# Kernel tuning notes

Measured on AMD Instinct MI355X. Metric: run time of the kernel, lower is better.

## Reference

```python
import jax, jax.numpy as jnp
import numpy as np

N = 524288   # total spokes
D = 128      # dim_hidden
B = 128      # graphs in batch
H = 64       # hubs per graph (static, num_hubs_type='S')
K = 4        # hubs_per_spoke


def setup_inputs() -> dict:
    key = jax.random.key(0)
    ks = jax.random.split(key, 5)
    x = jax.random.normal(ks[0], (N, D), jnp.float32)
    spoke_init_hub_idx = jax.random.randint(ks[1], (N,), 0, H)
    batch_idx = jnp.sort(jax.random.randint(ks[2], (N,), 0, B))
    s1 = 1.0 / np.sqrt(D)
    s2 = 1.0 / np.sqrt(2 * D)
    W1 = jax.random.uniform(ks[3], (D, 2 * D), jnp.float32, -s1, s1)
    b1 = jnp.zeros((2 * D,), jnp.float32)
    W2 = jax.random.uniform(ks[4], (2 * D, D), jnp.float32, -s2, s2)
    b2 = jnp.zeros((D,), jnp.float32)
    return {"x": x, "spoke_init_hub_idx": spoke_init_hub_idx, "batch_idx": batch_idx,
            "W1": W1, "b1": b1, "W2": W2, "b2": b2}


def reference(x, spoke_init_hub_idx, batch_idx, W1, b1, W2, b2):
    # FeedForward on spokes: Linear -> GELU(exact, torch default) -> Linear
    h = jax.nn.gelu(x @ W1 + b1, approximate=False) @ W2 + b2  # [N, D]

    # batched hub index: local hub idx offset by graph (uniform H hubs/graph)
    gidx = batch_idx * H + spoke_init_hub_idx  # [N]

    # scatter_mean of spoke features into hubs (empty hubs -> 0, as torch scatter_mean)
    sums = jax.ops.segment_sum(h, gidx, num_segments=B * H)                    # [B*H, D]
    cnt = jax.ops.segment_sum(jnp.ones((N,), h.dtype), gidx, num_segments=B * H)
    hub_features = sums / jnp.maximum(cnt, 1.0)[:, None]                       # [B*H, D]

    # assign each spoke to the K hubs closest to its initial hub (within its graph)
    hf = hub_features.reshape(B, H, D)
    d2 = jnp.sum((hf[:, :, None, :] - hf[:, None, :, :]) ** 2, axis=-1)        # [B, H, H]
    _, knn = jax.lax.top_k(-d2, K)                                             # [B, H, K] local hub ids
    hubs_idx = knn[batch_idx, spoke_init_hub_idx] + batch_idx[:, None] * H     # [N, K] global hub ids
    spokes_idx = jnp.repeat(jnp.arange(N), K)
    spokes_hubs_edge_index = jnp.stack([spokes_idx, hubs_idx.reshape(-1)], axis=0)  # [2, N*K]

    return hub_features, spokes_hubs_edge_index
```

## Files before the change

### kernel.cpp

```cpp
#include <hip/hip_runtime.h>
#include <hip/hip_bf16.h>

#define N_SPOKES 524288
#define DIM      128
#define DIM2     256
#define NB       128
#define NH       64
#define BH       8192

#define OUT_HF   0
#define OUT_E0   1048576
#define OUT_E1   3145728

typedef __attribute__((ext_vector_type(8))) short  short8;
typedef __attribute__((ext_vector_type(4))) float  float4v;
typedef __attribute__((ext_vector_type(4))) unsigned short ushort4v;

__device__ inline unsigned short f2bf(float f) {
    __hip_bfloat16 h = __float2bfloat16(f);
    return *reinterpret_cast<unsigned short*>(&h);
}

__device__ inline unsigned int pkbf(float a, float b) {
    __hip_bfloat162 h = __float22bfloat162_rn(make_float2(a, b));
    union { __hip_bfloat162 h; unsigned int u; } cv;
    cv.h = h;
    return cv.u;
}

__device__ inline float gelu_f(float v) {
    float s = v * (1.0f + 0.044715f * v * v);
    float e = __builtin_exp2f(-2.302118131f * s);
    return v * __builtin_amdgcn_rcpf(1.0f + e);
}

__global__ void setup_kernel(const int* __restrict__ batchidx, const int* __restrict__ hubidx,
                             const float* __restrict__ W1,
                             unsigned short* __restrict__ w1t,
                             int* __restrict__ goff, int* __restrict__ cnt) {
    int b = blockIdx.x, tid = threadIdx.x;
    if (b < 2048) {
        int i = b * 256 + tid;
        if (i < N_SPOKES) {
            int bi = batchidx[i];
            int bp = (i == 0) ? -1 : batchidx[i - 1];
            for (int g = bp + 1; g <= bi; ++g) goff[g] = i;
            if (i == N_SPOKES - 1)
                for (int g = bi + 1; g <= NB; ++g) goff[g] = N_SPOKES;
            atomicAdd(&cnt[bi * NH + hubidx[i]], 1);
        }
    } else {
        int idx = (b - 2048) * 256 + tid;
        if (idx < DIM * DIM2) {
            int n = idx >> 7, k = idx & 127;
            w1t[idx] = f2bf(W1[k * DIM2 + n]);
        }
    }
}

__launch_bounds__(512, 2)
__global__ void ffn_fused(const float* __restrict__ x,
                          const int* __restrict__ hubidx,
                          const int* __restrict__ goff,
                          const unsigned short* __restrict__ w1t,
                          const float* __restrict__ b1,
                          float* __restrict__ outbuf,
                          int atomic_mode) {
    __shared__ unsigned short sA[2][128 * 136];
    __shared__ unsigned short sU[256 * 40];
    __shared__ unsigned short sOne[2][64 * 136];

    const int tid  = threadIdx.x;
    const int lane = tid & 63;
    const int w    = tid >> 6;
    const int c_lo = lane & 15;
    const int c_hi = lane >> 4;
    const int wcb  = w * 32;
    const int g      = blockIdx.x >> 1;
    const int cchunk = blockIdx.x & 1;

    const int s = goff[g], e = goff[g + 1];
    const int len = e - s;
    const int cs  = (len + 1) >> 1;
    const int ms  = s + cchunk * cs;
    int me = ms + cs; if (me > e) me = e;
    const int n  = me - ms;
    const int nt = (n > 0) ? ((n + 127) >> 7) : 0;

    short8 bfr[2][4];
    #pragma unroll
    for (int n4 = 0; n4 < 2; ++n4)
        #pragma unroll
        for (int k = 0; k < 4; ++k) {
            int col = wcb + n4 * 16 + c_lo;
            bfr[n4][k] = *(const short8*)(w1t + col * DIM + k * 32 + c_hi * 8);
        }
    float bcol[2];
    #pragma unroll
    for (int n4 = 0; n4 < 2; ++n4) bcol[n4] = b1[wcb + n4 * 16 + c_lo];

    float4v hacc[4][2];
    #pragma unroll
    for (int mt = 0; mt < 4; ++mt)
        #pragma unroll
        for (int n4 = 0; n4 < 2; ++n4) hacc[mt][n4] = (float4v){0.f, 0.f, 0.f, 0.f};

    for (int i = tid; i < 4096; i += 512) {
        int b = i >> 11, r = (i >> 5) & 63, c = i & 31;
        *(unsigned long long*)&sOne[b][r * 136 + c * 4] = 0ULL;
    }

    const float4v* x4 = (const float4v*)x;

    float4v ld[8];
    int hub_nxt = -1;
    int hubA = -1, hubB = -1;
    if (nt > 0) {
        #pragma unroll
        for (int it = 0; it < 8; ++it) {
            int f = it * 512 + tid;
            int r = f >> 5;
            int rr = r < n ? r : n - 1;
            ld[it] = x4[(size_t)(ms + rr) * 32 + (f & 31)];
        }
        if (tid < 128) hub_nxt = (tid < n) ? hubidx[ms + tid] : -1;
    }
    __syncthreads();

    for (int t = 0; t < nt; ++t) {
        const int p = t & 1;
        const int hub_cur = hub_nxt;
        const int hclear  = p ? hubB : hubA;

        if (tid < 128) {
            if (hclear >= 0)  sOne[p][hclear * 136 + tid] = 0;
            if (hub_cur >= 0) sOne[p][hub_cur * 136 + tid] = (unsigned short)0x3F80;
        }
        if (p) hubB = hub_cur; else hubA = hub_cur;

        #pragma unroll
        for (int it = 0; it < 8; ++it) {
            int f = it * 512 + tid;
            int row = f >> 5, c4 = f & 31;
            float4v v = ld[it];
            unsigned int lo = pkbf(v.x, v.y);
            unsigned int hi = pkbf(v.z, v.w);
            *(uint2*)&sA[p][row * 136 + c4 * 4] = make_uint2(lo, hi);
        }
        __syncthreads();

        if (t + 1 < nt) {
            #pragma unroll
            for (int it = 0; it < 8; ++it) {
                int f = it * 512 + tid;
                int r = (t + 1) * 128 + (f >> 5);
                int rr = r < n ? r : n - 1;
                ld[it] = x4[(size_t)(ms + rr) * 32 + (f & 31)];
            }
            if (tid < 128) {
                int r = (t + 1) * 128 + tid;
                hub_nxt = (r < n) ? hubidx[ms + r] : -1;
            }
        }

        #pragma unroll
        for (int ks = 0; ks < 4; ++ks) {
            float4v acc[2][2];
            #pragma unroll
            for (int m2 = 0; m2 < 2; ++m2)
                #pragma unroll
                for (int n4 = 0; n4 < 2; ++n4) acc[m2][n4] = (float4v){0.f, 0.f, 0.f, 0.f};

            #pragma unroll
            for (int k = 0; k < 4; ++k)
                #pragma unroll
                for (int m2 = 0; m2 < 2; ++m2) {
                    short8 a = *(const short8*)&sA[p][(ks * 32 + m2 * 16 + c_lo) * 136 + k * 32 + c_hi * 8];
                    acc[m2][0] = __builtin_amdgcn_mfma_f32_16x16x32_bf16(a, bfr[0][k], acc[m2][0], 0, 0, 0);
                    acc[m2][1] = __builtin_amdgcn_mfma_f32_16x16x32_bf16(a, bfr[1][k], acc[m2][1], 0, 0, 0);
                }

            #pragma unroll
            for (int m2 = 0; m2 < 2; ++m2) {
                int rbase = m2 * 16 + c_hi * 4;
                #pragma unroll
                for (int n4 = 0; n4 < 2; ++n4) {
                    int col = wcb + n4 * 16 + c_lo;
                    float4v a4 = acc[m2][n4];
                    unsigned int lo = pkbf(gelu_f(a4.x + bcol[n4]), gelu_f(a4.y + bcol[n4]));
                    unsigned int hi = pkbf(gelu_f(a4.z + bcol[n4]), gelu_f(a4.w + bcol[n4]));
                    *(uint2*)&sU[col * 40 + rbase] = make_uint2(lo, hi);
                }
            }

            short8 aS[4];
            #pragma unroll
            for (int mt = 0; mt < 4; ++mt)
                aS[mt] = *(const short8*)&sOne[p][(mt * 16 + c_lo) * 136 + ks * 32 + c_hi * 8];
            short8 bU[2];
            #pragma unroll
            for (int n4 = 0; n4 < 2; ++n4)
                bU[n4] = *(const short8*)&sU[(wcb + n4 * 16 + c_lo) * 40 + c_hi * 8];
            #pragma unroll
            for (int mt = 0; mt < 4; ++mt)
                #pragma unroll
                for (int n4 = 0; n4 < 2; ++n4)
                    hacc[mt][n4] = __builtin_amdgcn_mfma_f32_16x16x32_bf16(aS[mt], bU[n4], hacc[mt][n4], 0, 0, 0);
        }
    }

    #pragma unroll
    for (int mt = 0; mt < 4; ++mt)
        #pragma unroll
        for (int n4 = 0; n4 < 2; ++n4) {
            float4v v = hacc[mt][n4];
            int col = wcb + n4 * 16 + c_lo;
            #pragma unroll
            for (int reg = 0; reg < 4; ++reg) {
                int hub = mt * 16 + c_hi * 4 + reg;
                size_t o = ((size_t)g * NH + hub) * DIM2 + col;
                if (atomic_mode) atomicAdd(&outbuf[o], v[reg]);
                else outbuf[(size_t)cchunk * BH * DIM2 + o] = v[reg];
            }
        }
}

__global__ void hubfeat_kernel(const float* __restrict__ part, int nchunk,
                               const int* __restrict__ cnt,
                               const float* __restrict__ W2, const float* __restrict__ b2,
                               float* __restrict__ out) {
    __shared__ float sSum[16 * 256];
    int tid = threadIdx.x;
    int d   = tid & 127;
    int hh  = tid >> 7;

    for (int i = tid; i < 16 * 256; i += 256) {
        size_t o = (size_t)(blockIdx.x * 16) * DIM2 + i;
        float v = 0.f;
        for (int c = 0; c < nchunk; ++c) v += part[(size_t)c * BH * DIM2 + o];
        sSum[i] = v;
    }
    __syncthreads();

    int h0 = hh * 8;
    float acc[8] = {0.f, 0.f, 0.f, 0.f, 0.f, 0.f, 0.f, 0.f};
    for (int k4 = 0; k4 < 64; ++k4) {
        float w0 = W2[(k4 * 4 + 0) * DIM + d];
        float w1 = W2[(k4 * 4 + 1) * DIM + d];
        float w2 = W2[(k4 * 4 + 2) * DIM + d];
        float w3 = W2[(k4 * 4 + 3) * DIM + d];
        #pragma unroll
        for (int j = 0; j < 8; ++j) {
            float4v sv = *(const float4v*)&sSum[(h0 + j) * 256 + k4 * 4];
            acc[j] += sv.x * w0 + sv.y * w1 + sv.z * w2 + sv.w * w3;
        }
    }
    float b2d = b2[d];
    #pragma unroll
    for (int j = 0; j < 8; ++j) {
        int h = blockIdx.x * 16 + h0 + j;
        float c = (float)cnt[h];
        out[OUT_HF + h * DIM + d] = (acc[j] + c * b2d) / fmaxf(c, 1.0f);
    }
}

__global__ void knn_edges(const float* __restrict__ hf, const int* __restrict__ goff,
                          const int* __restrict__ hubidx, float* __restrict__ out) {
    __shared__ float s[64 * 129];
    __shared__ float d2[64 * 64];
    __shared__ int sK[64 * 4];
    int g = blockIdx.x, tid = threadIdx.x;

    for (int i = tid; i < 64 * 128; i += 256) {
        int r = i >> 7, c = i & 127;
        s[r * 129 + c] = hf[OUT_HF + (g * 64 + r) * DIM + c];
    }
    __syncthreads();

    for (int p = tid; p < 4096; p += 256) {
        int i = p >> 6, j = p & 63;
        float a = 0.f;
        for (int k = 0; k < 128; ++k) {
            float dd = s[i * 129 + k] - s[j * 129 + k];
            a += dd * dd;
        }
        d2[p] = a;
    }
    __syncthreads();

    if (tid < 64) {
        float bv0 = 1e30f, bv1 = 1e30f, bv2 = 1e30f, bv3 = 1e30f;
        int   bi0 = 0,     bi1 = 0,     bi2 = 0,     bi3 = 0;
        for (int j = 0; j < 64; ++j) {
            float v = d2[tid * 64 + j];
            if (v < bv0)      { bv3=bv2; bi3=bi2; bv2=bv1; bi2=bi1; bv1=bv0; bi1=bi0; bv0=v; bi0=j; }
            else if (v < bv1) { bv3=bv2; bi3=bi2; bv2=bv1; bi2=bi1; bv1=v;   bi1=j; }
            else if (v < bv2) { bv3=bv2; bi3=bi2; bv2=v;   bi2=j; }
            else if (v < bv3) { bv3=v;   bi3=j; }
        }
        sK[tid * 4 + 0] = bi0; sK[tid * 4 + 1] = bi1;
        sK[tid * 4 + 2] = bi2; sK[tid * 4 + 3] = bi3;
    }
    __syncthreads();

    int sgs = goff[g], sge = goff[g + 1];
    float gbase = (float)(g * NH);
    for (int i = sgs + tid; i < sge; i += 256) {
        int h = hubidx[i];
        int4 kn = *(const int4*)&sK[h * 4];
        float fi = (float)i;
        float4v o0 = { fi, fi, fi, fi };
        ((float4v*)(out + OUT_E0))[i] = o0;
        float4v o1 = { kn.x + gbase, kn.y + gbase, kn.z + gbase, kn.w + gbase };
        ((float4v*)(out + OUT_E1))[i] = o1;
    }
}

extern "C" void kernel_launch(void* const* d_in, const int* in_sizes, int n_in,
                              void* d_out, int out_size, void* d_ws, size_t ws_size,
                              hipStream_t stream) {
    const float* x        = (const float*)d_in[0];
    const int*   hubidx   = (const int*)d_in[1];
    const int*   batchidx = (const int*)d_in[2];
    const float* W1       = (const float*)d_in[3];
    const float* b1       = (const float*)d_in[4];
    const float* W2       = (const float*)d_in[5];
    const float* b2       = (const float*)d_in[6];
    float* out = (float*)d_out;
    char*  ws  = (char*)d_ws;

    const size_t need_partial = 16879616;
    int atomic_mode = (ws_size < need_partial) ? 1 : 0;

    float*          part;
    int*            cnt;
    unsigned short* w1t;
    int*            goff;
    if (!atomic_mode) {
        part = (float*)ws;
        cnt  = (int*)(ws + 16777216);
        w1t  = (unsigned short*)(ws + 16809984);
        goff = (int*)(ws + 16875520);
    } else {
        part = (float*)ws;
        cnt  = (int*)(ws + 8388608);
        w1t  = (unsigned short*)(ws + 8421376);
        goff = (int*)(ws + 8486912);
    }

    (void)hipMemsetAsync(cnt, 0, 32768, stream);
    if (atomic_mode) (void)hipMemsetAsync(part, 0, 8388608, stream);

    setup_kernel<<<2176, 256, 0, stream>>>(batchidx, hubidx, W1, w1t, goff, cnt);
    ffn_fused   <<<256,  512, 0, stream>>>(x, hubidx, goff, w1t, b1, part, atomic_mode);
    hubfeat_kernel<<<512, 256, 0, stream>>>(part, atomic_mode ? 1 : 2, cnt, W2, b2, out);
    knn_edges   <<<NB,   256, 0, stream>>>(out, goff, hubidx, out);
}
```

Measured before the change: 492.8 us.

## Double ffn_fused threads to 1024 and register-tile knn distance computation

The fused FFN kernel now launches 1024 threads per block, with each of 16 waves owning 16 hidden columns instead of 32. This halves per-thread registers and the per-thread x loads, and puts more waves on the matrix units for each graph chunk. Separately, the knn pairwise-distance loop now loads the hub tile with float4 copies and has each thread compute a 4x4 register tile from vectorized shared-memory reads. The cost is more barrier participants per block and per-wave duplicate reads of the sOne tile.

```diff
diff --git a/kernel.cpp b/kernel.cpp
--- a/kernel.cpp
+++ b/kernel.cpp
@@ -58,7 +58,7 @@
     }
 }
 
-__launch_bounds__(512, 2)
+__launch_bounds__(1024, 4)
 __global__ void ffn_fused(const float* __restrict__ x,
                           const int* __restrict__ hubidx,
                           const int* __restrict__ goff,
@@ -75,7 +75,7 @@
     const int w    = tid >> 6;
     const int c_lo = lane & 15;
     const int c_hi = lane >> 4;
-    const int wcb  = w * 32;
+    const int wcb  = w * 16;
     const int g      = blockIdx.x >> 1;
     const int cchunk = blockIdx.x & 1;
 
@@ -87,38 +87,31 @@
     const int n  = me - ms;
     const int nt = (n > 0) ? ((n + 127) >> 7) : 0;
 
-    short8 bfr[2][4];
+    const int col = wcb + c_lo;
+    short8 bfr[4];
     #pragma unroll
-    for (int n4 = 0; n4 < 2; ++n4)
-        #pragma unroll
-        for (int k = 0; k < 4; ++k) {
-            int col = wcb + n4 * 16 + c_lo;
-            bfr[n4][k] = *(const short8*)(w1t + col * DIM + k * 32 + c_hi * 8);
-        }
-    float bcol[2];
+    for (int k = 0; k < 4; ++k)
+        bfr[k] = *(const short8*)(w1t + col * DIM + k * 32 + c_hi * 8);
+    const float bcol = b1[col];
+
+    float4v hacc[4];
     #pragma unroll
-    for (int n4 = 0; n4 < 2; ++n4) bcol[n4] = b1[wcb + n4 * 16 + c_lo];
-
-    float4v hacc[4][2];
-    #pragma unroll
-    for (int mt = 0; mt < 4; ++mt)
-        #pragma unroll
-        for (int n4 = 0; n4 < 2; ++n4) hacc[mt][n4] = (float4v){0.f, 0.f, 0.f, 0.f};
-
-    for (int i = tid; i < 4096; i += 512) {
+    for (int mt = 0; mt < 4; ++mt) hacc[mt] = (float4v){0.f, 0.f, 0.f, 0.f};
+
+    for (int i = tid; i < 4096; i += 1024) {
         int b = i >> 11, r = (i >> 5) & 63, c = i & 31;
         *(unsigned long long*)&sOne[b][r * 136 + c * 4] = 0ULL;
     }
 
     const float4v* x4 = (const float4v*)x;
 
-    float4v ld[8];
+    float4v ld[4];
     int hub_nxt = -1;
     int hubA = -1, hubB = -1;
     if (nt > 0) {
         #pragma unroll
-        for (int it = 0; it < 8; ++it) {
-            int f = it * 512 + tid;
+        for (int it = 0; it < 4; ++it) {
+            int f = it * 1024 + tid;
             int r = f >> 5;
             int rr = r < n ? r : n - 1;
             ld[it] = x4[(size_t)(ms + rr) * 32 + (f & 31)];
@@ -139,8 +132,8 @@
         if (p) hubB = hub_cur; else hubA = hub_cur;
 
         #pragma unroll
-        for (int it = 0; it < 8; ++it) {
-            int f = it * 512 + tid;
+        for (int it = 0; it < 4; ++it) {
+            int f = it * 1024 + tid;
             int row = f >> 5, c4 = f & 31;
             float4v v = ld[it];
             unsigned int lo = pkbf(v.x, v.y);
@@ -151,8 +144,8 @@
 
         if (t + 1 < nt) {
             #pragma unroll
-            for (int it = 0; it < 8; ++it) {
-                int f = it * 512 + tid;
+            for (int it = 0; it < 4; ++it) {
+                int f = it * 1024 + tid;
                 int r = (t + 1) * 128 + (f >> 5);
                 int rr = r < n ? r : n - 1;
                 ld[it] = x4[(size_t)(ms + rr) * 32 + (f & 31)];
@@ -165,64 +158,49 @@
 
         #pragma unroll
         for (int ks = 0; ks < 4; ++ks) {
-            float4v acc[2][2];
-            #pragma unroll
-            for (int m2 = 0; m2 < 2; ++m2)
-                #pragma unroll
-                for (int n4 = 0; n4 < 2; ++n4) acc[m2][n4] = (float4v){0.f, 0.f, 0.f, 0.f};
+            float4v acc[2];
+            acc[0] = (float4v){0.f, 0.f, 0.f, 0.f};
+            acc[1] = (float4v){0.f, 0.f, 0.f, 0.f};
 
             #pragma unroll
             for (int k = 0; k < 4; ++k)
                 #pragma unroll
                 for (int m2 = 0; m2 < 2; ++m2) {
                     short8 a = *(const short8*)&sA[p][(ks * 32 + m2 * 16 + c_lo) * 136 + k * 32 + c_hi * 8];
-                    acc[m2][0] = __builtin_amdgcn_mfma_f32_16x16x32_bf16(a, bfr[0][k], acc[m2][0], 0, 0, 0);
-                    acc[m2][1] = __builtin_amdgcn_mfma_f32_16x16x32_bf16(a, bfr[1][k], acc[m2][1], 0, 0, 0);
+                    acc[m2] = __builtin_amdgcn_mfma_f32_16x16x32_bf16(a, bfr[k], acc[m2], 0, 0, 0);
                 }
 
             #pragma unroll
             for (int m2 = 0; m2 < 2; ++m2) {
                 int rbase = m2 * 16 + c_hi * 4;
-                #pragma unroll
-                for (int n4 = 0; n4 < 2; ++n4) {
-                    int col = wcb + n4 * 16 + c_lo;
-                    float4v a4 = acc[m2][n4];
-                    unsigned int lo = pkbf(gelu_f(a4.x + bcol[n4]), gelu_f(a4.y + bcol[n4]));
-                    unsigned int hi = pkbf(gelu_f(a4.z + bcol[n4]), gelu_f(a4.w + bcol[n4]));
-                    *(uint2*)&sU[col * 40 + rbase] = make_uint2(lo, hi);
-                }
+                float4v a4 = acc[m2];
+                unsigned int lo = pkbf(gelu_f(a4.x + bcol), gelu_f(a4.y + bcol));
+                unsigned int hi = pkbf(gelu_f(a4.z + bcol), gelu_f(a4.w + bcol));
+                *(uint2*)&sU[col * 40 + rbase] = make_uint2(lo, hi);
             }
 
             short8 aS[4];
             #pragma unroll
             for (int mt = 0; mt < 4; ++mt)
                 aS[mt] = *(const short8*)&sOne[p][(mt * 16 + c_lo) * 136 + ks * 32 + c_hi * 8];
-            short8 bU[2];
-            #pragma unroll
-            for (int n4 = 0; n4 < 2; ++n4)
-                bU[n4] = *(const short8*)&sU[(wcb + n4 * 16 + c_lo) * 40 + c_hi * 8];
+            short8 bU = *(const short8*)&sU[col * 40 + c_hi * 8];
             #pragma unroll
             for (int mt = 0; mt < 4; ++mt)
-                #pragma unroll
-                for (int n4 = 0; n4 < 2; ++n4)
-                    hacc[mt][n4] = __builtin_amdgcn_mfma_f32_16x16x32_bf16(aS[mt], bU[n4], hacc[mt][n4], 0, 0, 0);
+                hacc[mt] = __builtin_amdgcn_mfma_f32_16x16x32_bf16(aS[mt], bU, hacc[mt], 0, 0, 0);
         }
     }
 
     #pragma unroll
-    for (int mt = 0; mt < 4; ++mt)
-        #pragma unroll
-        for (int n4 = 0; n4 < 2; ++n4) {
-            float4v v = hacc[mt][n4];
-            int col = wcb + n4 * 16 + c_lo;
-            #pragma unroll
-            for (int reg = 0; reg < 4; ++reg) {
-                int hub = mt * 16 + c_hi * 4 + reg;
-                size_t o = ((size_t)g * NH + hub) * DIM2 + col;
-                if (atomic_mode) atomicAdd(&outbuf[o], v[reg]);
-                else outbuf[(size_t)cchunk * BH * DIM2 + o] = v[reg];
-            }
-        }
+    for (int mt = 0; mt < 4; ++mt) {
+        float4v v = hacc[mt];
+        #pragma unroll
+        for (int reg = 0; reg < 4; ++reg) {
+            int hub = mt * 16 + c_hi * 4 + reg;
+            size_t o = ((size_t)g * NH + hub) * DIM2 + col;
+            if (atomic_mode) atomicAdd(&outbuf[o], v[reg]);
+            else outbuf[(size_t)cchunk * BH * DIM2 + o] = v[reg];
+        }
+    }
 }
 
 __global__ void hubfeat_kernel(const float* __restrict__ part, int nchunk,
@@ -266,25 +244,49 @@
 
 __global__ void knn_edges(const float* __restrict__ hf, const int* __restrict__ goff,
                           const int* __restrict__ hubidx, float* __restrict__ out) {
-    __shared__ float s[64 * 129];
+    __shared__ float s[64 * 132];
     __shared__ float d2[64 * 64];
     __shared__ int sK[64 * 4];
     int g = blockIdx.x, tid = threadIdx.x;
 
-    for (int i = tid; i < 64 * 128; i += 256) {
-        int r = i >> 7, c = i & 127;
-        s[r * 129 + c] = hf[OUT_HF + (g * 64 + r) * DIM + c];
-    }
-    __syncthreads();
-
-    for (int p = tid; p < 4096; p += 256) {
-        int i = p >> 6, j = p & 63;
-        float a = 0.f;
-        for (int k = 0; k < 128; ++k) {
-            float dd = s[i * 129 + k] - s[j * 129 + k];
-            a += dd * dd;
-        }
-        d2[p] = a;
+    for (int i = tid; i < 2048; i += 256) {
+        int r = i >> 5, c4 = i & 31;
+        *(float4v*)&s[r * 132 + c4 * 4] =
+            *(const float4v*)&hf[OUT_HF + (g * 64 + r) * DIM + c4 * 4];
+    }
+    __syncthreads();
+
+    {
+        int i0 = (tid >> 4) * 4;
+        int j0 = tid & 15;
+        float acc[4][4];
+        #pragma unroll
+        for (int a = 0; a < 4; ++a)
+            #pragma unroll
+            for (int b = 0; b < 4; ++b) acc[a][b] = 0.f;
+
+        for (int kc = 0; kc < 32; ++kc) {
+            float4v ai[4], bj[4];
+            #pragma unroll
+            for (int a = 0; a < 4; ++a) ai[a] = *(const float4v*)&s[(i0 + a) * 132 + kc * 4];
+            #pragma unroll
+            for (int b = 0; b < 4; ++b) bj[b] = *(const float4v*)&s[(j0 + b * 16) * 132 + kc * 4];
+            #pragma unroll
+            for (int a = 0; a < 4; ++a)
+                #pragma unroll
+                for (int b = 0; b < 4; ++b) {
+                    float d0 = ai[a].x - bj[b].x;
+                    float d1 = ai[a].y - bj[b].y;
+                    float dz = ai[a].z - bj[b].z;
+                    float d3 = ai[a].w - bj[b].w;
+                    acc[a][b] += d0 * d0 + d1 * d1 + dz * dz + d3 * d3;
+                }
+        }
+        #pragma unroll
+        for (int a = 0; a < 4; ++a)
+            #pragma unroll
+            for (int b = 0; b < 4; ++b)
+                d2[(i0 + a) * 64 + j0 + b * 16] = acc[a][b];
     }
     __syncthreads();
 
@@ -352,7 +354,7 @@
     if (atomic_mode) (void)hipMemsetAsync(part, 0, 8388608, stream);
 
     setup_kernel<<<2176, 256, 0, stream>>>(batchidx, hubidx, W1, w1t, goff, cnt);
-    ffn_fused   <<<256,  512, 0, stream>>>(x, hubidx, goff, w1t, b1, part, atomic_mode);
+    ffn_fused   <<<256, 1024, 0, stream>>>(x, hubidx, goff, w1t, b1, part, atomic_mode);
     hubfeat_kernel<<<512, 256, 0, stream>>>(part, atomic_mode ? 1 : 2, cnt, W2, b2, out);
     knn_edges   <<<NB,   256, 0, stream>>>(out, goff, hubidx, out);
 }
```

Measured after the change: 470.7 us. 4.5% less time.
